# Optimization experiments

Hardware: AMD Instinct MI355X
Metric: run time of the kernel (lower is better)

## Reference

```python
import jax, jax.numpy as jnp
import numpy as np

HEADS = 8
DIM_HEAD = 64
IMG = 32            # image_size
K = 5               # kernel_size
DIL = 1             # dilation
SEQ_LEN = 1279
SCALE = DIM_HEAD ** -0.5
IMG_SEQ = IMG * IMG                 # 1024
TEXT_LEN = SEQ_LEN + 1 - IMG_SEQ    # 256
NEG = -np.finfo(np.float32).max


def _unfold(img, pad_value):
    """torch F.unfold equivalent. img: [B, C, H, W] -> [B, H*W, K*K, C].
    Kernel-position index j is fastest-varying (matches torch unfold ordering
    after rearrange 'b (d j) i -> b i j d')."""
    B, C, H, W = img.shape
    p = ((K - 1) * DIL + 1) // 2
    padded = jnp.pad(img, ((0, 0), (0, 0), (p, p), (p, p)), constant_values=pad_value)
    patches = [padded[:, :, i * DIL:i * DIL + H, j * DIL:j * DIL + W]
               for i in range(K) for j in range(K)]
    pt = jnp.stack(patches, axis=2)            # [B, C, K*K, H, W]
    return pt.reshape(B, C, K * K, H * W).transpose(0, 3, 2, 1)


def _split_heads(t, b):
    # [b, N, h*d] -> [(b h), N, d]  (b slow, h fast)
    N = t.shape[1]
    return t.reshape(b, N, HEADS, DIM_HEAD).transpose(0, 2, 1, 3).reshape(b * HEADS, N, DIM_HEAD)


def setup_inputs() -> dict:
    key = jax.random.key(0)
    k1, k2, k3, k4 = jax.random.split(key, 4)
    dim = 512
    inner = HEADS * DIM_HEAD
    x = jax.random.normal(k1, (4, 1279, dim), dtype=jnp.float32)
    mask = jnp.ones((4, TEXT_LEN), dtype=bool)
    W_qkv = jax.random.normal(k2, (dim, inner * 3), dtype=jnp.float32) * 0.02
    W_out = jax.random.normal(k3, (inner, dim), dtype=jnp.float32) * 0.02
    b_out = jax.random.normal(k4, (dim,), dtype=jnp.float32) * 0.02
    return {"x": x, "mask": mask, "W_qkv": W_qkv, "W_out": W_out, "b_out": b_out}


def reference(x, mask, W_qkv, W_out, b_out):
    b, n, dim = x.shape
    pad = SEQ_LEN - n + 1
    xp = jnp.pad(x, ((0, 0), (0, pad), (0, 0)))            # [b, SEQ_LEN+1, dim]
    mask = mask[:, :TEXT_LEN]

    qkv = xp @ W_qkv
    q, k, v = jnp.split(qkv, 3, axis=-1)
    q = _split_heads(q, b) * SCALE                          # [(bh), N, d]
    k = _split_heads(k, b)
    v = _split_heads(v, b)

    q_text, q_img = q[:, :-IMG_SEQ], q[:, -IMG_SEQ:]
    k_text, k_img = k[:, :-IMG_SEQ], k[:, -IMG_SEQ:]
    v_text, v_img = v[:, :-IMG_SEQ], v[:, -IMG_SEQ:]

    # ---- text-to-text causal attention ----
    dots_text = jnp.einsum('bid,bjd->bij', q_text, k_text)
    tl = TEXT_LEN
    text_causal = jnp.triu(jnp.ones((tl, tl), dtype=bool), 1)
    dots_text = jnp.where(text_causal[None], NEG, dots_text)
    attn_text = jax.nn.softmax(dots_text, axis=-1)
    out_text = jnp.einsum('bij,bjd->bid', attn_text, v_text)

    # ---- local-window image attention (unfold) ----
    bh = b * HEADS
    k_img2 = k_img.reshape(bh, IMG, IMG, DIM_HEAD).transpose(0, 3, 1, 2)
    v_img2 = v_img.reshape(bh, IMG, IMG, DIM_HEAD).transpose(0, 3, 1, 2)
    k_imgu = _unfold(k_img2, 0.0)                           # [(bh), IMG_SEQ, K*K, d]
    v_imgu = _unfold(v_img2, 0.0)

    dots_image = jnp.einsum('bid,bijd->bij', q_img, k_imgu)         # [(bh), IMG_SEQ, K*K]
    dots_i2t = jnp.einsum('bid,bjd->bij', q_img, k_text)            # [(bh), IMG_SEQ, tl]

    # causal mask over local window via unfolded position indices
    idx = jnp.arange(IMG_SEQ, dtype=jnp.float32).reshape(1, 1, IMG, IMG)
    k_idx = _unfold(idx, float(IMG_SEQ))[..., 0]            # [1, IMG_SEQ, K*K]
    q_idx = jnp.arange(IMG_SEQ, dtype=jnp.float32)[None, :, None]
    causal_mask = q_idx < k_idx                             # [1, IMG_SEQ, K*K]

    text_pad_mask = jnp.repeat(~mask, HEADS, axis=0)[:, None, :]    # [(bh), 1, tl]
    full_mask = jnp.concatenate([
        jnp.broadcast_to(text_pad_mask, (bh, IMG_SEQ, tl)),
        jnp.broadcast_to(causal_mask, (bh, IMG_SEQ, K * K)),
    ], axis=-1)

    dots = jnp.concatenate([dots_i2t, dots_image], axis=-1)
    dots = jnp.where(full_mask, NEG, dots)
    attn = jax.nn.softmax(dots, axis=-1)
    attn_i2t, attn_img = attn[..., :tl], attn[..., tl:]

    out_image = (jnp.einsum('bij,bijd->bid', attn_img, v_imgu)
                 + jnp.einsum('bij,bjd->bid', attn_i2t, v_text))

    # ---- merge and project ----
    out = jnp.concatenate([out_text, out_image], axis=1)    # [(bh), N, d]
    N = out.shape[1]
    out = out.reshape(b, HEADS, N, DIM_HEAD).transpose(0, 2, 1, 3).reshape(b, N, HEADS * DIM_HEAD)
    out = out @ W_out + b_out
    return out[:, :n]
```

## Files before the change

kernel.cpp:

```cpp
#include <hip/hip_runtime.h>
#include <hip/hip_bf16.h>
#include <math.h>

#define HEADS   8
#define DH      64
#define IMGW    32
#define KKER    5
#define SEQ     1280
#define NTOK    1279
#define TL      256
#define IMG_SEQ 1024
#define DIM     512
#define BATCH   4
#define BH      32
#define SCALE   0.125f
#define QSCALE  (0.125f * 1.44269504088896f)
#define NEGB    (-1.0e30f)

#define WQN  (DIM * 3 * DIM)
#define WON  (DIM * DIM)
#define QKVN ((size_t)BH * SEQ * DH)
#define AON  ((size_t)BATCH * SEQ * DIM)

#define XPBLK   1280
#define WQTILES 768
#define WOTILES 256


typedef unsigned short u16;
typedef __attribute__((ext_vector_type(8))) short bf16x8;
typedef __attribute__((ext_vector_type(4))) short bf16x4;
typedef __attribute__((ext_vector_type(4))) float f32x4;

__device__ inline u16 f2b(float f) {
    unsigned int u = __float_as_uint(f);
    return (u16)((u + 0x7FFFu + ((u >> 16) & 1u)) >> 16);
}
__device__ inline unsigned pack2(float a, float b) {
    return (unsigned)f2b(a) | ((unsigned)f2b(b) << 16);
}

__device__ inline void ldsload16(const u16* g, u16* l) {
    __builtin_amdgcn_global_load_lds(
        (const __attribute__((address_space(1))) unsigned int*)g,
        (__attribute__((address_space(3))) unsigned int*)l, 16, 0, 0);
}

__device__ inline void lds_barrier() {
    asm volatile("s_waitcnt lgkmcnt(0)\n\ts_barrier" ::: "memory");
}

__global__ __launch_bounds__(256) void cvt_all(
    const float* __restrict__ x, const float* __restrict__ Wq,
    const float* __restrict__ Wo, u16* __restrict__ xbf,
    u16* __restrict__ WqT, u16* __restrict__ WoT)
{
    __shared__ u16 tile[32][33];
    const int b = blockIdx.x;
    if (b < XPBLK) {
        const int i = b * 256 + threadIdx.x;
        const int row = i >> 6;
        const int bb = row / SEQ, nn = row % SEQ;
        union { unsigned u[4]; bf16x8 v; } r;
        if (nn < NTOK) {
            const size_t j = ((size_t)(bb * NTOK + nn) * 128 + (i & 63) * 2);
            const float4 a = ((const float4*)x)[j];
            const float4 c = ((const float4*)x)[j + 1];
            r.u[0] = pack2(a.x, a.y); r.u[1] = pack2(a.z, a.w);
            r.u[2] = pack2(c.x, c.y); r.u[3] = pack2(c.z, c.w);
        } else {
            r.u[0] = r.u[1] = r.u[2] = r.u[3] = 0u;
        }
        ((bf16x8*)xbf)[i] = r.v;
        return;
    }
    int t = b - XPBLK;
    const float* src; u16* dst; int C;
    if (t < WQTILES) { src = Wq; dst = WqT; C = 3 * DIM; }
    else             { t -= WQTILES; src = Wo; dst = WoT; C = DIM; }
    const int tc = C / 32;
    const int tr0 = (t / tc) * 32, tc0 = (t % tc) * 32;
    const int ty = threadIdx.x >> 5, tx = threadIdx.x & 31;
    #pragma unroll
    for (int s = 0; s < 4; s++) {
        const int r = ty + 8 * s;
        tile[r][tx] = f2b(src[(size_t)(tr0 + r) * C + tc0 + tx]);
    }
    __syncthreads();
    #pragma unroll
    for (int s = 0; s < 4; s++) {
        const int c = ty + 8 * s;
        dst[(size_t)(tc0 + c) * DIM + tr0 + tx] = tile[tx][c];
    }
}

__global__ __launch_bounds__(256) void qkv_mfma6(
    const u16* __restrict__ xbf, const u16* __restrict__ WqT,
    u16* __restrict__ Qbf, u16* __restrict__ Ktl, u16* __restrict__ Vtl)
{
    __shared__ u16 pool[12288];
    u16* const buf0 = pool;
    u16* const buf1 = pool + 6144;
    const int tid  = threadIdx.x;
    const int lane = tid & 63, wave = tid >> 6;
    const int quad = lane >> 4, l16 = lane & 15;
    const int wm = (wave >> 1) * 32, wn = (wave & 1) * 64;

    const int id  = blockIdx.x;
    const int nid = (id & 7) * 120 + (id >> 3);
    const int m0 = (nid / 12) * 64, n0 = (nid % 12) * 128;

    const u16* ga  = xbf + (size_t)(m0 + (tid >> 2)) * DIM + (tid & 3) * 8;
    const u16* gb0 = WqT + (size_t)(n0 + (tid >> 2)) * DIM + (tid & 3) * 8;
    const u16* gb1 = WqT + (size_t)(n0 + 64 + (tid >> 2)) * DIM + (tid & 3) * 8;

    f32x4 acc[2][4];
    #pragma unroll
    for (int i = 0; i < 2; i++)
        #pragma unroll
        for (int j = 0; j < 4; j++) acc[i][j] = (f32x4){0.f, 0.f, 0.f, 0.f};

    auto stage = [&](u16* b, int k) {
        ldsload16(ga  + k, b + wave * 512);
        ldsload16(gb0 + k, b + 2048 + wave * 512);
        ldsload16(gb1 + k, b + 4096 + wave * 512);
    };
    auto comp = [&](const u16* b) {
        bf16x8 af_[2], bf_[4];
        #pragma unroll
        for (int i = 0; i < 2; i++)
            af_[i] = *(const bf16x8*)&b[(wm + i * 16 + l16) * 32 + quad * 8];
        #pragma unroll
        for (int j = 0; j < 4; j++)
            bf_[j] = *(const bf16x8*)&b[2048 + (wn + j * 16 + l16) * 32 + quad * 8];
        #pragma unroll
        for (int i = 0; i < 2; i++)
            #pragma unroll
            for (int j = 0; j < 4; j++)
                acc[i][j] = __builtin_amdgcn_mfma_f32_16x16x32_bf16(
                    af_[i], bf_[j], acc[i][j], 0, 0, 0);
    };

    stage(buf0, 0);
    stage(buf1, 32);
    #pragma unroll
    for (int s = 0; s < 16; s++) {
        if (s == 15) asm volatile("s_waitcnt vmcnt(0)" ::: "memory");
        else         asm volatile("s_waitcnt vmcnt(3)" ::: "memory");
        __builtin_amdgcn_s_barrier();
        comp((s & 1) ? buf1 : buf0);
        asm volatile("s_waitcnt lgkmcnt(0)" ::: "memory");
        __builtin_amdgcn_sched_barrier(0);
        __builtin_amdgcn_s_barrier();
        if (s < 14) stage((s & 1) ? buf1 : buf0, 32 * (s + 2));
    }

    const int which = n0 >> 9;
    const float scl = (which == 0) ? QSCALE : 1.f;
    #pragma unroll
    for (int i = 0; i < 2; i++)
        #pragma unroll
        for (int r = 0; r < 4; r++)
            #pragma unroll
            for (int j = 0; j < 4; j++)
                pool[(wm + i * 16 + quad * 4 + r) * 144 + wn + j * 16 + l16] =
                    f2b(acc[i][j][r] * scl);
    __syncthreads();

    const int b_  = m0 / SEQ;
    const int nn0 = m0 % SEQ;
    if (which == 0) {
        #pragma unroll
        for (int s = 0; s < 4; s++) {
            const int c   = tid + 256 * s;
            const int row = c >> 4, c8 = (c & 15) * 8;
            const int col511 = (n0 + c8) & 511;
            const int h = col511 >> 6, d0 = col511 & 63;
            const int bhh = b_ * HEADS + h;
            const bf16x8 v = *(const bf16x8*)&pool[row * 144 + c8];
            *(bf16x8*)&Qbf[((size_t)bhh * SEQ + nn0 + row) * DH + d0] = v;
        }
    } else if (which == 1) {
        #pragma unroll
        for (int s = 0; s < 4; s++) {
            const int c   = tid + 256 * s;
            const int row = c >> 4, c8 = (c & 15) * 8;
            const int col511 = (n0 + c8) & 511;
            const int h = col511 >> 6, d0 = col511 & 63;
            const int bhh = b_ * HEADS + h;
            const int key = nn0 + row;
            const bf16x8 v = *(const bf16x8*)&pool[row * 144 + c8];
            *(bf16x8*)&Ktl[(size_t)bhh * 81920 +
                (size_t)((((key >> 4) * 2 + (d0 >> 5)) * 512) +
                         ((key & 15) + 16 * ((d0 >> 3) & 3)) * 8)] = v;
        }
    } else {
        #pragma unroll
        for (int s = 0; s < 4; s++) {
            const int c   = tid + 256 * s;
            const int col = c & 127, r8 = (c >> 7) * 8;
            const int col511 = (n0 + col) & 511;
            const int h = col511 >> 6, d = col511 & 63;
            const int bhh = b_ * HEADS + h;
            const int key0 = nn0 + r8;
            union { u16 u[8]; bf16x8 v; } w;
            #pragma unroll
            for (int k = 0; k < 8; k++)
                w.u[k] = pool[(r8 + k) * 144 + col];
            *(bf16x8*)&Vtl[(size_t)bhh * 81920 +
                (size_t)((((key0 >> 5) * 4 + (d >> 4)) * 512) +
                         ((d & 15) + 16 * ((r8 >> 3) & 3)) * 8)] = w.v;
        }
    }
}

__global__ __launch_bounds__(256, 6) void attn_fused(
    const u16* __restrict__ Qbf, const u16* __restrict__ Ktl,
    const u16* __restrict__ Vtl, u16* __restrict__ AObf)
{
    const int id = blockIdx.x;
    const int bh = (id & 7) | (((id >> 3) & 3) << 3);
    const int bx = id >> 5;
    const bool istext = bx < 16;
    const int it = bx - 16;
    const int r0 = it >> 1;
    const int qt0 = istext ? bx * 16 : it * 16;
    const int qrow0 = istext ? qt0 : TL + qt0;
    const int tid = threadIdx.x;
    const int lane = tid & 63, wave = tid >> 6;
    const int quad = lane >> 4, l16 = lane & 15;

    __shared__ float Opool[4][1088];
    __shared__ float msm[4][16];
    __shared__ float mss[4][16];

    const int krs = istext ? 0 : min(max(r0 - 2, 0), IMGW - 5);
    const int cbase = TL + krs * 32;
    const bool tactive = !istext || (4 * wave <= bx);
    const bool xtra = (!istext) && (wave == 0);

    u16* const Pw = (u16*)Opool[wave];

    const u16* qr = Qbf + ((size_t)bh * SEQ + qrow0 + l16) * DH;
    const bf16x8 af0 = *(const bf16x8*)(qr + quad * 8);
    const bf16x8 af1 = *(const bf16x8*)(qr + 32 + quad * 8);

    const u16* kt = Ktl + (size_t)bh * 81920;

    f32x4 sacc[4], cacc[2], xacc[2];
    #pragma unroll
    for (int j = 0; j < 4; j++) sacc[j] = (f32x4){0.f, 0.f, 0.f, 0.f};
    #pragma unroll
    for (int s = 0; s < 2; s++) {
        cacc[s] = (f32x4){0.f, 0.f, 0.f, 0.f};
        xacc[s] = (f32x4){0.f, 0.f, 0.f, 0.f};
    }

    if (tactive) {
        bf16x8 kf0[4], kf1[4];
        #pragma unroll
        for (int j = 0; j < 4; j++) {
            kf0[j] = *(const bf16x8*)&kt[(size_t)(((wave * 4 + j) * 2) * 512) + lane * 8];
            kf1[j] = *(const bf16x8*)&kt[(size_t)(((wave * 4 + j) * 2 + 1) * 512) + lane * 8];
        }
        #pragma unroll
        for (int j = 0; j < 4; j++) {
            sacc[j] = __builtin_amdgcn_mfma_f32_16x16x32_bf16(af0, kf0[j], sacc[j], 0, 0, 0);
            sacc[j] = __builtin_amdgcn_mfma_f32_16x16x32_bf16(af1, kf1[j], sacc[j], 0, 0, 0);
        }
    }
    if (!istext) {
        const int cb16 = cbase >> 4;
        {
            bf16x8 cf0[2], cf1[2];
            #pragma unroll
            for (int s = 0; s < 2; s++) {
                const int blk = cb16 + 2 * wave + s;
                cf0[s] = *(const bf16x8*)&kt[(size_t)((blk * 2) * 512) + lane * 8];
                cf1[s] = *(const bf16x8*)&kt[(size_t)((blk * 2 + 1) * 512) + lane * 8];
            }
            #pragma unroll
            for (int s = 0; s < 2; s++) {
                cacc[s] = __builtin_amdgcn_mfma_f32_16x16x32_bf16(af0, cf0[s], cacc[s], 0, 0, 0);
                cacc[s] = __builtin_amdgcn_mfma_f32_16x16x32_bf16(af1, cf1[s], cacc[s], 0, 0, 0);
            }
        }
        if (xtra) {
            bf16x8 cf0[2], cf1[2];
            #pragma unroll
            for (int s = 0; s < 2; s++) {
                const int blk = cb16 + 8 + s;
                cf0[s] = *(const bf16x8*)&kt[(size_t)((blk * 2) * 512) + lane * 8];
                cf1[s] = *(const bf16x8*)&kt[(size_t)((blk * 2 + 1) * 512) + lane * 8];
            }
            #pragma unroll
            for (int s = 0; s < 2; s++) {
                xacc[s] = __builtin_amdgcn_mfma_f32_16x16x32_bf16(af0, cf0[s], xacc[s], 0, 0, 0);
                xacc[s] = __builtin_amdgcn_mfma_f32_16x16x32_bf16(af1, cf1[s], xacc[s], 0, 0, 0);
            }
        }
    }

    float m4[4];
    #pragma unroll
    for (int r = 0; r < 4; r++) {
        const int q = quad * 4 + r;
        float m = NEGB;
        if (istext) {
            if (tactive) {
                const int qg = qt0 + q;
                #pragma unroll
                for (int j = 0; j < 4; j++) {
                    const int key = wave * 64 + j * 16 + l16;
                    const float v = (key <= qg) ? sacc[j][r] : NEGB;
                    sacc[j][r] = v;
                    m = fmaxf(m, v);
                }
            }
        } else {
            const int qi = qt0 + q;
            #pragma unroll
            for (int j = 0; j < 4; j++) m = fmaxf(m, sacc[j][r]);
            #pragma unroll
            for (int s = 0; s < 2; s++) {
                const int t = 2 * wave + s;
                const int kidx = krs * 32 + t * 16 + l16;
                const int kr = kidx >> 5, kc = kidx & 31;
                const bool valid = (abs(kr - r0) <= 2) && (abs(kc - qi % 32) <= 2)
                                   && (kidx <= qi);
                const float v = valid ? cacc[s][r] : NEGB;
                cacc[s][r] = v;
                m = fmaxf(m, v);
            }
            if (xtra) {
                #pragma unroll
                for (int s = 0; s < 2; s++) {
                    const int t = 8 + s;
                    const int kidx = krs * 32 + t * 16 + l16;
                    const int kr = kidx >> 5, kc = kidx & 31;
                    const bool valid = (abs(kr - r0) <= 2) && (abs(kc - qi % 32) <= 2)
                                       && (kidx <= qi);
                    const float v = valid ? xacc[s][r] : NEGB;
                    xacc[s][r] = v;
                    m = fmaxf(m, v);
                }
            }
        }
        m4[r] = m;
    }
    #pragma unroll
    for (int off = 1; off < 16; off <<= 1)
        #pragma unroll
        for (int r = 0; r < 4; r++)
            m4[r] = fmaxf(m4[r], __shfl_xor(m4[r], off));

    float s4[4];
    #pragma unroll
    for (int r = 0; r < 4; r++) {
        const int q = quad * 4 + r;
        const float mr = m4[r];
        float s = 0.f;
        if (tactive) {
            #pragma unroll
            for (int j = 0; j < 4; j++) {
                const float p = exp2f(sacc[j][r] - mr);
                Pw[q * 136 + j * 16 + l16] = f2b(p);
                s += p;
            }
        }
        if (!istext) {
            #pragma unroll
            for (int ss = 0; ss < 2; ss++) {
                const float p = exp2f(cacc[ss][r] - mr);
                Pw[q * 136 + 64 + ss * 16 + l16] = f2b(p);
                s += p;
            }
            if (xtra) {
                #pragma unroll
                for (int ss = 0; ss < 2; ss++) {
                    const float p = exp2f(xacc[ss][r] - mr);
                    Pw[q * 136 + 96 + ss * 16 + l16] = f2b(p);
                    s += p;
                }
            }
        }
        s4[r] = s;
    }
    #pragma unroll
    for (int off = 1; off < 16; off <<= 1)
        #pragma unroll
        for (int r = 0; r < 4; r++)
            s4[r] += __shfl_xor(s4[r], off);
    if (l16 == 0)
        #pragma unroll
        for (int r = 0; r < 4; r++) {
            msm[wave][quad * 4 + r] = m4[r];
            mss[wave][quad * 4 + r] = s4[r];
        }
    asm volatile("s_waitcnt lgkmcnt(0)" ::: "memory");

    bool cact[4];
    int ck[4];
    ck[0] = wave * 64; ck[1] = wave * 64 + 32;
    ck[2] = cbase + wave * 32; ck[3] = cbase + 128;
    if (istext) {
        cact[0] = tactive;
        cact[1] = (bx >= 4 * wave + 2);
        cact[2] = false; cact[3] = false;
    } else {
        cact[0] = cact[1] = cact[2] = true; cact[3] = (wave == 0);
    }

    const u16* vt = Vtl + (size_t)bh * 81920;
    f32x4 o2[4];
    #pragma unroll
    for (int j = 0; j < 4; j++) o2[j] = (f32x4){0.f, 0.f, 0.f, 0.f};

    #pragma unroll
    for (int c = 0; c < 4; c++) {
        if (cact[c]) {
            const bf16x8 av = *(const bf16x8*)&Pw[l16 * 136 + c * 32 + quad * 8];
            const int kcb = (ck[c] >> 5) * 4;
            bf16x8 bv[4];
            #pragma unroll
            for (int j = 0; j < 4; j++)
                bv[j] = *(const bf16x8*)&vt[(size_t)((kcb + j) * 512) + lane * 8];
            #pragma unroll
            for (int j = 0; j < 4; j++)
                o2[j] = __builtin_amdgcn_mfma_f32_16x16x32_bf16(av, bv[j], o2[j], 0, 0, 0);
        }
    }

    #pragma unroll
    for (int j = 0; j < 4; j++)
        #pragma unroll
        for (int r = 0; r < 4; r++)
            Opool[wave][(quad * 4 + r) * 68 + j * 16 + l16] = o2[j][r];

    lds_barrier();

    const int qq = tid >> 4, d4 = (tid & 15) * 4;
    const float mm = fmaxf(fmaxf(msm[0][qq], msm[1][qq]),
                           fmaxf(msm[2][qq], msm[3][qq]));
    float wgt[4];
    float den = 0.f;
    #pragma unroll
    for (int w = 0; w < 4; w++) {
        wgt[w] = exp2f(msm[w][qq] - mm);
        den += mss[w][qq] * wgt[w];
    }
    float o[4];
    #pragma unroll
    for (int e = 0; e < 4; e++) o[e] = 0.f;
    #pragma unroll
    for (int w = 0; w < 4; w++) {
        const float* Ow = &Opool[w][qq * 68 + d4];
        #pragma unroll
        for (int e = 0; e < 4; e++) o[e] += Ow[e] * wgt[w];
    }
    const float inv = 1.f / den;
    union { u16 u[4]; bf16x4 v; } pk;
    #pragma unroll
    for (int e = 0; e < 4; e++) pk.u[e] = f2b(o[e] * inv);
    const int b_ = bh >> 3, h = bh & 7;
    *(bf16x4*)&AObf[((size_t)b_ * SEQ + qrow0 + qq) * DIM + h * DH + d4] = pk.v;
}

__global__ __launch_bounds__(256) void proj_mfma6(
    const u16* __restrict__ AObf, const u16* __restrict__ WoT,
    const float* __restrict__ bias, float* __restrict__ out)
{
    __shared__ u16 pool[10240];
    u16* const buf0 = pool;
    u16* const buf1 = pool + 5120;
    const int tid  = threadIdx.x;
    const int lane = tid & 63, wave = tid >> 6;
    const int quad = lane >> 4, l16 = lane & 15;
    const int wm = (wave >> 1) * 16, wn = (wave & 1) * 64;

    const int id  = blockIdx.x;
    const int nid = (id & 7) * 80 + (id >> 3);
    const int m0 = (nid / 4) * 32, n0 = (nid % 4) * 128;

    const u16* ga  = AObf + (size_t)(m0 + ((tid & 127) >> 2)) * DIM + (tid & 3) * 8;
    const u16* gb0 = WoT + (size_t)(n0 + (tid >> 2)) * DIM + (tid & 3) * 8;
    const u16* gb1 = WoT + (size_t)(n0 + 64 + (tid >> 2)) * DIM + (tid & 3) * 8;

    f32x4 acc[4];
    #pragma unroll
    for (int j = 0; j < 4; j++) acc[j] = (f32x4){0.f, 0.f, 0.f, 0.f};

    auto stage = [&](u16* b, int k) {
        if (wave < 2) ldsload16(ga + k, b + (wave & 1) * 512);
        ldsload16(gb0 + k, b + 1024 + wave * 512);
        ldsload16(gb1 + k, b + 3072 + wave * 512);
    };
    auto comp = [&](const u16* b) {
        const bf16x8 af = *(const bf16x8*)&b[(wm + l16) * 32 + quad * 8];
        bf16x8 bf_[4];
        #pragma unroll
        for (int j = 0; j < 4; j++)
            bf_[j] = *(const bf16x8*)&b[1024 + (wn + j * 16 + l16) * 32 + quad * 8];
        #pragma unroll
        for (int j = 0; j < 4; j++)
            acc[j] = __builtin_amdgcn_mfma_f32_16x16x32_bf16(af, bf_[j], acc[j], 0, 0, 0);
    };

    stage(buf0, 0);
    stage(buf1, 32);
    #pragma unroll
    for (int s = 0; s < 16; s++) {
        if (s == 15)        asm volatile("s_waitcnt vmcnt(0)" ::: "memory");
        else if (wave < 2)  asm volatile("s_waitcnt vmcnt(3)" ::: "memory");
        else                asm volatile("s_waitcnt vmcnt(2)" ::: "memory");
        __builtin_amdgcn_s_barrier();
        comp((s & 1) ? buf1 : buf0);
        asm volatile("s_waitcnt lgkmcnt(0)" ::: "memory");
        __builtin_amdgcn_sched_barrier(0);
        __builtin_amdgcn_s_barrier();
        if (s < 14) stage((s & 1) ? buf1 : buf0, 32 * (s + 2));
    }

    #pragma unroll
    for (int r = 0; r < 4; r++) {
        const int mm = m0 + wm + quad * 4 + r;
        const int bb = mm / SEQ, nn = mm % SEQ;
        if (nn >= NTOK) continue;
        const size_t mr = (size_t)(bb * NTOK + nn);
        #pragma unroll
        for (int j = 0; j < 4; j++) {
            const int ncol = n0 + wn + j * 16 + l16;
            out[mr * DIM + ncol] = acc[j][r] + bias[ncol];
        }
    }
}

extern "C" void kernel_launch(void* const* d_in, const int* in_sizes, int n_in,
                              void* d_out, int out_size, void* d_ws, size_t ws_size,
                              hipStream_t stream)
{
    const float* x    = (const float*)d_in[0];
    const float* Wqkv = (const float*)d_in[2];
    const float* Wout = (const float*)d_in[3];
    const float* bout = (const float*)d_in[4];
    float* out = (float*)d_out;

    u16* wsu  = (u16*)d_ws;
    u16* xbf  = wsu;
    u16* WqT  = xbf + AON;
    u16* WoT  = WqT + WQN;
    u16* Qbf  = WoT + WON;
    u16* Ktl  = Qbf + QKVN;
    u16* Vtl  = Ktl + QKVN;
    u16* AObf = Vtl + QKVN;

    cvt_all   <<<XPBLK + WQTILES + WOTILES, 256, 0, stream>>>(x, Wqkv, Wout, xbf, WqT, WoT);
    qkv_mfma6 <<<dim3(960), 256, 0, stream>>>(xbf, WqT, Qbf, Ktl, Vtl);
    attn_fused<<<dim3(80 * BH), 256, 0, stream>>>(Qbf, Ktl, Vtl, AObf);
    proj_mfma6<<<dim3(640), 256, 0, stream>>>(AObf, WoT, bout, out);
}
```

Measured before the change: 115.2 us.

## Enlarge QKV GEMM tile to 128x128 and hoist attention mask index math

The QKV projection kernel moves from 64x128 to 128x128 output tiles. Each wave now computes a 64x64 sub-tile (4x4 MFMAs) and the grid is halved to 480 blocks, which raises arithmetic intensity and reduces redundant loads of the weight matrix. LDS use grows and fewer blocks may lower occupancy and wave balance across CUs. In the attention kernel, the Q fragment loads are skipped for inactive text waves, and the per-key row, column and range checks for the local-window mask are hoisted out of the per-row loop.

```diff
diff --git a/kernel.cpp b/kernel.cpp
--- a/kernel.cpp
+++ b/kernel.cpp
@@ -94,47 +94,47 @@
     }
 }
 
-__global__ __launch_bounds__(256) void qkv_mfma6(
+__global__ __launch_bounds__(256) void qkv_mfma7(
     const u16* __restrict__ xbf, const u16* __restrict__ WqT,
     u16* __restrict__ Qbf, u16* __restrict__ Ktl, u16* __restrict__ Vtl)
 {
-    __shared__ u16 pool[12288];
+    __shared__ u16 pool[17408];
     u16* const buf0 = pool;
-    u16* const buf1 = pool + 6144;
+    u16* const buf1 = pool + 8192;
     const int tid  = threadIdx.x;
     const int lane = tid & 63, wave = tid >> 6;
     const int quad = lane >> 4, l16 = lane & 15;
-    const int wm = (wave >> 1) * 32, wn = (wave & 1) * 64;
+    const int wr = (wave >> 1) * 64, wc = (wave & 1) * 64;
 
     const int id  = blockIdx.x;
-    const int nid = (id & 7) * 120 + (id >> 3);
-    const int m0 = (nid / 12) * 64, n0 = (nid % 12) * 128;
-
-    const u16* ga  = xbf + (size_t)(m0 + (tid >> 2)) * DIM + (tid & 3) * 8;
-    const u16* gb0 = WqT + (size_t)(n0 + (tid >> 2)) * DIM + (tid & 3) * 8;
-    const u16* gb1 = WqT + (size_t)(n0 + 64 + (tid >> 2)) * DIM + (tid & 3) * 8;
-
-    f32x4 acc[2][4];
-    #pragma unroll
-    for (int i = 0; i < 2; i++)
+    const int nid = (id & 7) * 60 + (id >> 3);
+    const int m0 = (nid / 12) * 128, n0 = (nid % 12) * 128;
+
+    const u16* ga = xbf + (size_t)(m0 + (tid >> 2)) * DIM + (tid & 3) * 8;
+    const u16* gb = WqT + (size_t)(n0 + (tid >> 2)) * DIM + (tid & 3) * 8;
+
+    f32x4 acc[4][4];
+    #pragma unroll
+    for (int i = 0; i < 4; i++)
         #pragma unroll
         for (int j = 0; j < 4; j++) acc[i][j] = (f32x4){0.f, 0.f, 0.f, 0.f};
 
     auto stage = [&](u16* b, int k) {
-        ldsload16(ga  + k, b + wave * 512);
-        ldsload16(gb0 + k, b + 2048 + wave * 512);
-        ldsload16(gb1 + k, b + 4096 + wave * 512);
+        ldsload16(ga + k,            b + wave * 512);
+        ldsload16(ga + 64 * DIM + k, b + 2048 + wave * 512);
+        ldsload16(gb + k,            b + 4096 + wave * 512);
+        ldsload16(gb + 64 * DIM + k, b + 6144 + wave * 512);
     };
     auto comp = [&](const u16* b) {
-        bf16x8 af_[2], bf_[4];
-        #pragma unroll
-        for (int i = 0; i < 2; i++)
-            af_[i] = *(const bf16x8*)&b[(wm + i * 16 + l16) * 32 + quad * 8];
+        bf16x8 af_[4], bf_[4];
+        #pragma unroll
+        for (int i = 0; i < 4; i++)
+            af_[i] = *(const bf16x8*)&b[(wr + i * 16 + l16) * 32 + quad * 8];
         #pragma unroll
         for (int j = 0; j < 4; j++)
-            bf_[j] = *(const bf16x8*)&b[2048 + (wn + j * 16 + l16) * 32 + quad * 8];
-        #pragma unroll
-        for (int i = 0; i < 2; i++)
+            bf_[j] = *(const bf16x8*)&b[4096 + (wc + j * 16 + l16) * 32 + quad * 8];
+        #pragma unroll
+        for (int i = 0; i < 4; i++)
             #pragma unroll
             for (int j = 0; j < 4; j++)
                 acc[i][j] = __builtin_amdgcn_mfma_f32_16x16x32_bf16(
@@ -146,7 +146,7 @@
     #pragma unroll
     for (int s = 0; s < 16; s++) {
         if (s == 15) asm volatile("s_waitcnt vmcnt(0)" ::: "memory");
-        else         asm volatile("s_waitcnt vmcnt(3)" ::: "memory");
+        else         asm volatile("s_waitcnt vmcnt(4)" ::: "memory");
         __builtin_amdgcn_s_barrier();
         comp((s & 1) ? buf1 : buf0);
         asm volatile("s_waitcnt lgkmcnt(0)" ::: "memory");
@@ -158,12 +158,12 @@
     const int which = n0 >> 9;
     const float scl = (which == 0) ? QSCALE : 1.f;
     #pragma unroll
-    for (int i = 0; i < 2; i++)
+    for (int i = 0; i < 4; i++)
         #pragma unroll
         for (int r = 0; r < 4; r++)
             #pragma unroll
             for (int j = 0; j < 4; j++)
-                pool[(wm + i * 16 + quad * 4 + r) * 144 + wn + j * 16 + l16] =
+                pool[(wr + i * 16 + quad * 4 + r) * 136 + wc + j * 16 + l16] =
                     f2b(acc[i][j][r] * scl);
     __syncthreads();
 
@@ -171,32 +171,32 @@
     const int nn0 = m0 % SEQ;
     if (which == 0) {
         #pragma unroll
-        for (int s = 0; s < 4; s++) {
+        for (int s = 0; s < 8; s++) {
             const int c   = tid + 256 * s;
             const int row = c >> 4, c8 = (c & 15) * 8;
             const int col511 = (n0 + c8) & 511;
             const int h = col511 >> 6, d0 = col511 & 63;
             const int bhh = b_ * HEADS + h;
-            const bf16x8 v = *(const bf16x8*)&pool[row * 144 + c8];
+            const bf16x8 v = *(const bf16x8*)&pool[row * 136 + c8];
             *(bf16x8*)&Qbf[((size_t)bhh * SEQ + nn0 + row) * DH + d0] = v;
         }
     } else if (which == 1) {
         #pragma unroll
-        for (int s = 0; s < 4; s++) {
+        for (int s = 0; s < 8; s++) {
             const int c   = tid + 256 * s;
             const int row = c >> 4, c8 = (c & 15) * 8;
             const int col511 = (n0 + c8) & 511;
             const int h = col511 >> 6, d0 = col511 & 63;
             const int bhh = b_ * HEADS + h;
             const int key = nn0 + row;
-            const bf16x8 v = *(const bf16x8*)&pool[row * 144 + c8];
+            const bf16x8 v = *(const bf16x8*)&pool[row * 136 + c8];
             *(bf16x8*)&Ktl[(size_t)bhh * 81920 +
                 (size_t)((((key >> 4) * 2 + (d0 >> 5)) * 512) +
                          ((key & 15) + 16 * ((d0 >> 3) & 3)) * 8)] = v;
         }
     } else {
         #pragma unroll
-        for (int s = 0; s < 4; s++) {
+        for (int s = 0; s < 8; s++) {
             const int c   = tid + 256 * s;
             const int col = c & 127, r8 = (c >> 7) * 8;
             const int col511 = (n0 + col) & 511;
@@ -206,7 +206,7 @@
             union { u16 u[8]; bf16x8 v; } w;
             #pragma unroll
             for (int k = 0; k < 8; k++)
-                w.u[k] = pool[(r8 + k) * 144 + col];
+                w.u[k] = pool[(r8 + k) * 136 + col];
             *(bf16x8*)&Vtl[(size_t)bhh * 81920 +
                 (size_t)((((key0 >> 5) * 4 + (d >> 4)) * 512) +
                          ((d & 15) + 16 * ((r8 >> 3) & 3)) * 8)] = w.v;
@@ -241,9 +241,12 @@
 
     u16* const Pw = (u16*)Opool[wave];
 
-    const u16* qr = Qbf + ((size_t)bh * SEQ + qrow0 + l16) * DH;
-    const bf16x8 af0 = *(const bf16x8*)(qr + quad * 8);
-    const bf16x8 af1 = *(const bf16x8*)(qr + 32 + quad * 8);
+    bf16x8 af0, af1;
+    if (tactive) {
+        const u16* qr = Qbf + ((size_t)bh * SEQ + qrow0 + l16) * DH;
+        af0 = *(const bf16x8*)(qr + quad * 8);
+        af1 = *(const bf16x8*)(qr + 32 + quad * 8);
+    }
 
     const u16* kt = Ktl + (size_t)bh * 81920;
 
@@ -301,6 +304,19 @@
         }
     }
 
+    int  kidx_c[2], kc_c[2], kidx_x[2], kc_x[2];
+    bool krok_c[2], krok_x[2];
+    if (!istext) {
+        #pragma unroll
+        for (int s = 0; s < 2; s++) {
+            kidx_c[s] = krs * 32 + (2 * wave + s) * 16 + l16;
+            kc_c[s]   = kidx_c[s] & 31;
+            krok_c[s] = (abs((kidx_c[s] >> 5) - r0) <= 2);
+            kidx_x[s] = krs * 32 + (8 + s) * 16 + l16;
+            kc_x[s]   = kidx_x[s] & 31;
+            krok_x[s] = (abs((kidx_x[s] >> 5) - r0) <= 2);
+        }
+    }
     float m4[4];
     #pragma unroll
     for (int r = 0; r < 4; r++) {
@@ -319,15 +335,13 @@
             }
         } else {
             const int qi = qt0 + q;
+            const int qcol = qi & 31;
             #pragma unroll
             for (int j = 0; j < 4; j++) m = fmaxf(m, sacc[j][r]);
             #pragma unroll
             for (int s = 0; s < 2; s++) {
-                const int t = 2 * wave + s;
-                const int kidx = krs * 32 + t * 16 + l16;
-                const int kr = kidx >> 5, kc = kidx & 31;
-                const bool valid = (abs(kr - r0) <= 2) && (abs(kc - qi % 32) <= 2)
-                                   && (kidx <= qi);
+                const bool valid = krok_c[s] && (abs(kc_c[s] - qcol) <= 2)
+                                   && (kidx_c[s] <= qi);
                 const float v = valid ? cacc[s][r] : NEGB;
                 cacc[s][r] = v;
                 m = fmaxf(m, v);
@@ -335,11 +349,8 @@
             if (xtra) {
                 #pragma unroll
                 for (int s = 0; s < 2; s++) {
-                    const int t = 8 + s;
-                    const int kidx = krs * 32 + t * 16 + l16;
-                    const int kr = kidx >> 5, kc = kidx & 31;
-                    const bool valid = (abs(kr - r0) <= 2) && (abs(kc - qi % 32) <= 2)
-                                       && (kidx <= qi);
+                    const bool valid = krok_x[s] && (abs(kc_x[s] - qcol) <= 2)
+                                       && (kidx_x[s] <= qi);
                     const float v = valid ? xacc[s][r] : NEGB;
                     xacc[s][r] = v;
                     m = fmaxf(m, v);
@@ -555,7 +566,7 @@
     u16* AObf = Vtl + QKVN;
 
     cvt_all   <<<XPBLK + WQTILES + WOTILES, 256, 0, stream>>>(x, Wqkv, Wout, xbf, WqT, WoT);
-    qkv_mfma6 <<<dim3(960), 256, 0, stream>>>(xbf, WqT, Qbf, Ktl, Vtl);
+    qkv_mfma7 <<<dim3(480), 256, 0, stream>>>(xbf, WqT, Qbf, Ktl, Vtl);
     attn_fused<<<dim3(80 * BH), 256, 0, stream>>>(Qbf, Ktl, Vtl, AObf);
     proj_mfma6<<<dim3(640), 256, 0, stream>>>(AObf, WoT, bout, out);
 }
```

After: 113.1 us. No clear change (-1.8%).
